# Performance work log

Measured on AMD Instinct MI355X. Metric: run time of the kernel, lower is better.

The kernel has to match this reference:

```python
import jax, jax.numpy as jnp
import numpy as np

K_NEAREST = 5
EPS = 1e-6


def setup_inputs() -> dict:
    key = jax.random.key(0)
    k1, k2, k3 = jax.random.split(key, 3)
    N_Q, N_DB, D_OUT, D_AUX = 4096, 65536, 32, 32
    return {
        "embedding_features": jax.random.normal(k1, (N_Q, D_OUT), dtype=jnp.float32),
        "db_embedding": jax.random.normal(k2, (N_DB, D_OUT), dtype=jnp.float32),
        "auxiliary_features": jax.random.normal(k3, (N_DB, D_AUX), dtype=jnp.float32),
    }


def reference(embedding_features, db_embedding, auxiliary_features):
    d_out = embedding_features.shape[-1]
    q = embedding_features.reshape(-1, d_out)          # [Nq, D]
    db = db_embedding.reshape(-1, d_out)               # [Ndb, D]

    # Euclidean cdist via the expanded quadratic form (same math as torch.cdist p=2).
    q_sq = jnp.sum(q * q, axis=1, keepdims=True)       # [Nq, 1]
    db_sq = jnp.sum(db * db, axis=1)[None, :]          # [1, Ndb]
    dist_sq = q_sq + db_sq - 2.0 * (q @ db.T)          # [Nq, Ndb]
    distances = jnp.sqrt(jnp.maximum(dist_sq, 0.0))

    # k smallest distances == k largest of negated distances.
    neg_top, nearest_indices = jax.lax.top_k(-distances, K_NEAREST)  # [Nq, k]
    nearest_distances = -neg_top                                      # [Nq, k]

    aux = auxiliary_features.reshape(-1, auxiliary_features.shape[-1])
    nearest_aux = aux[nearest_indices]                 # [Nq, k, Daux]

    weights = 1.0 / (nearest_distances + EPS)
    weights = weights / jnp.sum(weights, axis=1, keepdims=True)

    return jnp.sum(nearest_aux * weights[..., None], axis=1)  # [Nq, Daux]
```

## Files before the change

kernel.cpp:

```cpp
#include <hip/hip_runtime.h>
#include <math.h>

#define N_Q   4096
#define N_DB  65536
#define DIM   32
#define KNN   5
#define NC    64
#define CH    (N_DB / NC)
#define NSUB  32
#define NCAND (NC * 6)
#define BIAS  256.0f

typedef _Float16 half8  __attribute__((ext_vector_type(8)));
typedef __fp16   fp16x2 __attribute__((ext_vector_type(2)));
typedef float floatx16  __attribute__((ext_vector_type(16)));

union H8  { half8 h; uint4 u4; unsigned u[4]; };
union F16 { floatx16 v; float4 q4[4]; unsigned w[16]; };
union HU  { fp16x2 h2; unsigned u; };

__device__ __forceinline__ unsigned cvt2(float a, float b) {
    HU t; t.h2 = __builtin_amdgcn_cvt_pkrtz(a, b);
    return t.u;
}

__device__ __forceinline__ void gl4(uint4& d, unsigned long long a) {
    asm volatile("global_load_dwordx4 %0, %1, off" : "=v"(d) : "v"(a) : "memory");
}
__device__ __forceinline__ void gl4_1024(uint4& d, unsigned long long a) {
    asm volatile("global_load_dwordx4 %0, %1, off offset:1024" : "=v"(d) : "v"(a) : "memory");
}
__device__ __forceinline__ void gl1(unsigned& d, unsigned long long a) {
    asm volatile("global_load_dword %0, %1, off" : "=v"(d) : "v"(a) : "memory");
}
#define VMWAIT6 do { asm volatile("s_waitcnt vmcnt(6)" ::: "memory"); \
                     __builtin_amdgcn_sched_barrier(0); } while (0)

__global__ __launch_bounds__(256) void k_prep(const float* __restrict__ DB,
                                              uint4* __restrict__ DBh,
                                              unsigned* __restrict__ DBn) {
    int p = blockIdx.x * 256 + threadIdx.x;
    const float4* src = (const float4*)(DB + (size_t)p * DIM);
    float4 f[8]; float s = 0.f;
#pragma unroll
    for (int j = 0; j < 8; ++j) {
        f[j] = src[j];
        s += f[j].x * f[j].x + f[j].y * f[j].y + f[j].z * f[j].z + f[j].w * f[j].w;
    }
    float v  = BIAS - 0.5f * s;
    float hi = (float)(__fp16)v;
    float lo = v - hi;
    DBn[p] = cvt2(hi, lo);
    int t = p >> 5, r = p & 31;
#pragma unroll
    for (int gi = 0; gi < 4; ++gi) {
        uint4 g;
        g.x = cvt2(f[2 * gi].x, f[2 * gi].y);
        g.y = cvt2(f[2 * gi].z, f[2 * gi].w);
        g.z = cvt2(f[2 * gi + 1].x, f[2 * gi + 1].y);
        g.w = cvt2(f[2 * gi + 1].z, f[2 * gi + 1].w);
        DBh[(size_t)t * 128 + gi * 32 + r] = g;
    }
}

__global__ __launch_bounds__(256, 4) void k_scan(const float* __restrict__ Q,
                                                 const uint4* __restrict__ DBh,
                                                 const unsigned* __restrict__ DBn,
                                                 unsigned* __restrict__ cand) {
    const int tid = threadIdx.x, lane = tid & 63, w = tid >> 6;
    const int h = lane >> 5, row = lane & 31;
    const int chunk = blockIdx.x & (NC - 1);
    const int qb    = blockIdx.x >> 6;
    const int q     = qb * 128 + w * 32 + row;
    const int pbase = chunk * CH;

    const float* qp = Q + (size_t)q * DIM;
    float4 qa = *(const float4*)(qp + h * 8);
    float4 qb4 = *(const float4*)(qp + h * 8 + 4);
    float4 qc = *(const float4*)(qp + 16 + h * 8);
    float4 qd = *(const float4*)(qp + 16 + h * 8 + 4);
    H8 b1, b2, b3;
    b1.u[0] = cvt2(qa.x, qa.y);   b1.u[1] = cvt2(qa.z, qa.w);
    b1.u[2] = cvt2(qb4.x, qb4.y); b1.u[3] = cvt2(qb4.z, qb4.w);
    b2.u[0] = cvt2(qc.x, qc.y);   b2.u[1] = cvt2(qc.z, qc.w);
    b2.u[2] = cvt2(qd.x, qd.y);   b2.u[3] = cvt2(qd.z, qd.w);
    b3.u[0] = (h == 0) ? cvt2(1.f, 1.f) : 0u;
    b3.u[1] = 0u; b3.u[2] = 0u; b3.u[3] = 0u;
    const unsigned hmask = (h == 0) ? 0xFFFFFFFFu : 0u;

    unsigned maskv;
    asm("v_mov_b32 %0, 0xFFFFFC00" : "=v"(maskv));

    const unsigned long long abase_u =
        (unsigned long long)(DBh + (size_t)(pbase >> 5) * 128 + h * 32 + row);
    const unsigned long long nbase_u =
        (unsigned long long)(DBn + pbase + row);

    floatx16 zc;
#pragma unroll
    for (int r = 0; r < 16; ++r) zc[r] = 0.f;

    float tk[6];
#pragma unroll
    for (int r = 0; r < 6; ++r) tk[r] = 0.f;

    constexpr int ROWC[16] = {0,1,2,3, 8,9,10,11, 16,17,18,19, 24,25,26,27};

    auto compute = [&](const H8& A1, const H8& A2, unsigned A3u, const int s) {
        H8 a3;
        a3.u[0] = A3u & hmask;
        a3.u[1] = 0u; a3.u[2] = 0u; a3.u[3] = 0u;
        floatx16 acc = __builtin_amdgcn_mfma_f32_32x32x16_f16(a3.h, b3.h, zc, 0, 0, 0);
        acc = __builtin_amdgcn_mfma_f32_32x32x16_f16(A1.h, b1.h, acc, 0, 0, 0);
        acc = __builtin_amdgcn_mfma_f32_32x32x16_f16(A2.h, b2.h, acc, 0, 0, 0);
        F16 pk; pk.v = acc;
        const int meta = s << 5;
        float p[16];
#pragma unroll
        for (int r = 0; r < 16; ++r)
            p[r] = __uint_as_float((pk.w[r] & maskv) | (unsigned)(meta | ROWC[r]));
        float hi8[8], lo8[8];
#pragma unroll
        for (int i = 0; i < 8; ++i) { hi8[i] = fmaxf(p[2*i], p[2*i+1]); lo8[i] = fminf(p[2*i], p[2*i+1]); }
        float H4[4], L4[4];
#pragma unroll
        for (int i = 0; i < 4; ++i) {
            H4[i] = fmaxf(hi8[2*i], hi8[2*i+1]);
            L4[i] = fmaxf(fmaxf(lo8[2*i], lo8[2*i+1]), fminf(hi8[2*i], hi8[2*i+1]));
        }
        float H2[2], L2[2];
#pragma unroll
        for (int i = 0; i < 2; ++i) {
            H2[i] = fmaxf(H4[2*i], H4[2*i+1]);
            L2[i] = fmaxf(fmaxf(L4[2*i], L4[2*i+1]), fminf(H4[2*i], H4[2*i+1]));
        }
        float c1 = fmaxf(H2[0], H2[1]);
        float c2 = fmaxf(fmaxf(L2[0], L2[1]), fminf(H2[0], H2[1]));
        {
            float m01 = fminf(tk[0], c1), m02 = fminf(tk[1], c1);
            float m03 = fminf(tk[2], c1), m04 = fminf(tk[3], c1);
            float m05 = fminf(tk[4], c1);
            float m12 = fminf(tk[0], c2), m13 = fminf(tk[1], c2);
            float m14 = fminf(tk[2], c2), m15 = fminf(tk[3], c2);
            tk[0] = fmaxf(tk[0], c1);
            tk[1] = fmaxf(fmaxf(tk[1], m01), c2);
            tk[2] = fmaxf(fmaxf(tk[2], m02), m12);
            tk[3] = fmaxf(fmaxf(tk[3], m03), m13);
            tk[4] = fmaxf(fmaxf(tk[4], m04), m14);
            tk[5] = fmaxf(fmaxf(tk[5], m05), m15);
        }
    };

    auto LD = [&](H8& x1, H8& x2, unsigned& x3, const int s) {
        const unsigned long long a = abase_u + (unsigned long long)s * 2048ull;
        gl4(x1.u4, a);
        gl4_1024(x2.u4, a);
        gl1(x3, nbase_u + (unsigned long long)s * 128ull);
    };

    H8 sA1, sA2, sB1, sB2, sC1, sC2, sD1, sD2;
    unsigned nA, nB, nC, nD;
    LD(sA1, sA2, nA, 0);
    LD(sB1, sB2, nB, 1);
    for (int s = 0; s < NSUB; s += 4) {
        LD(sC1, sC2, nC, s + 2);
        VMWAIT6; compute(sA1, sA2, nA, s);
        LD(sD1, sD2, nD, s + 3);
        VMWAIT6; compute(sB1, sB2, nB, s + 1);
        LD(sA1, sA2, nA, s + 4);
        VMWAIT6; compute(sC1, sC2, nC, s + 2);
        LD(sB1, sB2, nB, s + 5);
        VMWAIT6; compute(sD1, sD2, nD, s + 3);
    }

#pragma unroll
    for (int r = 0; r < 6; ++r)
        tk[r] = __uint_as_float(__float_as_uint(tk[r]) | (unsigned)(h << 2));

    float other[6];
#pragma unroll
    for (int i = 0; i < 6; ++i) other[i] = __shfl_xor(tk[i], 32, 64);
#pragma unroll
    for (int i = 0; i < 6; ++i) {
        float val = other[i];
#pragma unroll
        for (int j = 0; j < 6; ++j) { float mx = fmaxf(tk[j], val); val = fminf(tk[j], val); tk[j] = mx; }
    }
    if (h == 0) {
        unsigned* dst = cand + ((size_t)q * NC + chunk) * 6;
#pragma unroll
        for (int r = 0; r < 6; ++r) dst[r] = __float_as_uint(tk[r]);
    }
}

__global__ __launch_bounds__(256) void k_merge(const float* __restrict__ Q,
                                               const float* __restrict__ DB,
                                               const float* __restrict__ AUX,
                                               const unsigned* __restrict__ cand,
                                               float* __restrict__ out) {
    const int tid = threadIdx.x, lane = tid & 63, w = tid >> 6;
    const int q = blockIdx.x * 4 + w;

    const unsigned* cq = cand + (size_t)q * NCAND + (size_t)lane * 6;
    float cur[6];
#pragma unroll
    for (int r = 0; r < 6; ++r) cur[r] = __uint_as_float(cq[r]);

    float wv[12]; int wl[12];
#pragma unroll
    for (int r = 0; r < 12; ++r) {
        float bv = cur[0]; int bl = lane;
#pragma unroll
        for (int off = 32; off >= 1; off >>= 1) {
            float ov = __shfl_xor(bv, off, 64);
            int   ol = __shfl_xor(bl, off, 64);
            if (ov > bv || (ov == bv && ol < bl)) { bv = ov; bl = ol; }
        }
        wv[r] = bv; wl[r] = bl;
        if (bl == lane) {
#pragma unroll
            for (int s = 0; s < 5; ++s) cur[s] = cur[s + 1];
            cur[5] = -1.f;
        }
    }

    float dist = 1e30f; int dbi = 0x7fffffff;
    if (lane < 12) {
        unsigned u = __float_as_uint(wv[lane]) & 1023u;
        dbi = wl[lane] * CH + (int)u;
        const float4* dp = (const float4*)(DB + (size_t)dbi * DIM);
        const float4* qp = (const float4*)(Q + (size_t)q * DIM);
        float dot = 0.f, qs = 0.f, ds = 0.f;
#pragma unroll
        for (int j = 0; j < DIM / 4; ++j) {
            float4 a = qp[j], d = dp[j];
            dot += a.x * d.x + a.y * d.y + a.z * d.z + a.w * d.w;
            qs  += a.x * a.x + a.y * a.y + a.z * a.z + a.w * a.w;
            ds  += d.x * d.x + d.y * d.y + d.z * d.z + d.w * d.w;
        }
        dist = sqrtf(fmaxf(qs + ds - 2.f * dot, 0.f));
    }
    float wd[KNN]; int wi[KNN];
#pragma unroll
    for (int r = 0; r < KNN; ++r) {
        float bd = dist; int bi = dbi;
#pragma unroll
        for (int off = 32; off >= 1; off >>= 1) {
            float od = __shfl_xor(bd, off, 64);
            int   oi = __shfl_xor(bi, off, 64);
            if (od < bd || (od == bd && oi < bi)) { bd = od; bi = oi; }
        }
        wd[r] = bd; wi[r] = bi;
        if (dist == bd && dbi == bi) dist = 1e30f;
    }
    float ww[KNN], W = 0.f;
#pragma unroll
    for (int r = 0; r < KNN; ++r) { ww[r] = 1.f / (wd[r] + 1e-6f); W += ww[r]; }
    if (lane < DIM) {
        float o = 0.f;
#pragma unroll
        for (int r = 0; r < KNN; ++r) o += ww[r] * AUX[(size_t)wi[r] * DIM + lane];
        out[(size_t)q * DIM + lane] = o / W;
    }
}

extern "C" void kernel_launch(void* const* d_in, const int* in_sizes, int n_in,
                              void* d_out, int out_size, void* d_ws, size_t ws_size,
                              hipStream_t stream) {
    const float* Q   = (const float*)d_in[0];
    const float* DB  = (const float*)d_in[1];
    const float* AUX = (const float*)d_in[2];
    float* out = (float*)d_out;

    char* ws = (char*)d_ws;
    uint4*    DBh = (uint4*)ws;                         ws += (size_t)(N_DB / 32) * 128 * 16;
    unsigned* DBn = (unsigned*)ws;                      ws += (size_t)N_DB * 4;
    unsigned* cand = (unsigned*)ws;

    k_prep<<<N_DB / 256, 256, 0, stream>>>(DB, DBh, DBn);
    k_scan<<<(N_Q / 128) * NC, 256, 0, stream>>>(Q, DBh, DBn, cand);
    k_merge<<<N_Q / 4, 256, 0, stream>>>(Q, DB, AUX, cand, out);
}
```

Before: 139.9 us.

## Hand-write top-2 merge in inline asm and shrink load pipeline depth

```diff
diff --git a/kernel.cpp b/kernel.cpp
--- a/kernel.cpp
+++ b/kernel.cpp
@@ -33,7 +33,7 @@
 __device__ __forceinline__ void gl1(unsigned& d, unsigned long long a) {
     asm volatile("global_load_dword %0, %1, off" : "=v"(d) : "v"(a) : "memory");
 }
-#define VMWAIT6 do { asm volatile("s_waitcnt vmcnt(6)" ::: "memory"); \
+#define VMWAIT3 do { asm volatile("s_waitcnt vmcnt(3)" ::: "memory"); \
                      __builtin_amdgcn_sched_barrier(0); } while (0)
 
 __global__ __launch_bounds__(256) void k_prep(const float* __restrict__ DB,
@@ -114,41 +114,74 @@
         acc = __builtin_amdgcn_mfma_f32_32x32x16_f16(A1.h, b1.h, acc, 0, 0, 0);
         acc = __builtin_amdgcn_mfma_f32_32x32x16_f16(A2.h, b2.h, acc, 0, 0, 0);
         F16 pk; pk.v = acc;
-        const int meta = s << 5;
-        float p[16];
+        const unsigned meta = (unsigned)(s << 5);
+        unsigned p[16];
 #pragma unroll
         for (int r = 0; r < 16; ++r)
-            p[r] = __uint_as_float((pk.w[r] & maskv) | (unsigned)(meta | ROWC[r]));
-        float hi8[8], lo8[8];
-#pragma unroll
-        for (int i = 0; i < 8; ++i) { hi8[i] = fmaxf(p[2*i], p[2*i+1]); lo8[i] = fminf(p[2*i], p[2*i+1]); }
-        float H4[4], L4[4];
-#pragma unroll
-        for (int i = 0; i < 4; ++i) {
-            H4[i] = fmaxf(hi8[2*i], hi8[2*i+1]);
-            L4[i] = fmaxf(fmaxf(lo8[2*i], lo8[2*i+1]), fminf(hi8[2*i], hi8[2*i+1]));
-        }
-        float H2[2], L2[2];
-#pragma unroll
-        for (int i = 0; i < 2; ++i) {
-            H2[i] = fmaxf(H4[2*i], H4[2*i+1]);
-            L2[i] = fmaxf(fmaxf(L4[2*i], L4[2*i+1]), fminf(H4[2*i], H4[2*i+1]));
-        }
-        float c1 = fmaxf(H2[0], H2[1]);
-        float c2 = fmaxf(fmaxf(L2[0], L2[1]), fminf(H2[0], H2[1]));
-        {
-            float m01 = fminf(tk[0], c1), m02 = fminf(tk[1], c1);
-            float m03 = fminf(tk[2], c1), m04 = fminf(tk[3], c1);
-            float m05 = fminf(tk[4], c1);
-            float m12 = fminf(tk[0], c2), m13 = fminf(tk[1], c2);
-            float m14 = fminf(tk[2], c2), m15 = fminf(tk[3], c2);
-            tk[0] = fmaxf(tk[0], c1);
-            tk[1] = fmaxf(fmaxf(tk[1], m01), c2);
-            tk[2] = fmaxf(fmaxf(tk[2], m02), m12);
-            tk[3] = fmaxf(fmaxf(tk[3], m03), m13);
-            tk[4] = fmaxf(fmaxf(tk[4], m04), m14);
-            tk[5] = fmaxf(fmaxf(tk[5], m05), m15);
-        }
+            p[r] = (pk.w[r] & maskv) | (meta | (unsigned)ROWC[r]);
+        float q0, q1, q2, q3, T0, T1, T2, T3, U0, U1, U2, U3;
+        asm(
+            "v_max_f32 %[q0], %[p0], %[p1]\n\t"
+            "v_min_f32 %[q1], %[p0], %[p1]\n\t"
+            "v_max_f32 %[q2], %[p2], %[p3]\n\t"
+            "v_min_f32 %[q3], %[p2], %[p3]\n\t"
+            "v_max_f32 %[T0], %[q0], %[q2]\n\t"
+            "v_min_f32 %[U0], %[q0], %[q2]\n\t"
+            "v_max3_f32 %[U0], %[q1], %[q3], %[U0]\n\t"
+            "v_max_f32 %[q0], %[p4], %[p5]\n\t"
+            "v_min_f32 %[q1], %[p4], %[p5]\n\t"
+            "v_max_f32 %[q2], %[p6], %[p7]\n\t"
+            "v_min_f32 %[q3], %[p6], %[p7]\n\t"
+            "v_max_f32 %[T1], %[q0], %[q2]\n\t"
+            "v_min_f32 %[U1], %[q0], %[q2]\n\t"
+            "v_max3_f32 %[U1], %[q1], %[q3], %[U1]\n\t"
+            "v_max_f32 %[q0], %[p8], %[p9]\n\t"
+            "v_min_f32 %[q1], %[p8], %[p9]\n\t"
+            "v_max_f32 %[q2], %[p10], %[p11]\n\t"
+            "v_min_f32 %[q3], %[p10], %[p11]\n\t"
+            "v_max_f32 %[T2], %[q0], %[q2]\n\t"
+            "v_min_f32 %[U2], %[q0], %[q2]\n\t"
+            "v_max3_f32 %[U2], %[q1], %[q3], %[U2]\n\t"
+            "v_max_f32 %[q0], %[p12], %[p13]\n\t"
+            "v_min_f32 %[q1], %[p12], %[p13]\n\t"
+            "v_max_f32 %[q2], %[p14], %[p15]\n\t"
+            "v_min_f32 %[q3], %[p14], %[p15]\n\t"
+            "v_max_f32 %[T3], %[q0], %[q2]\n\t"
+            "v_min_f32 %[U3], %[q0], %[q2]\n\t"
+            "v_max3_f32 %[U3], %[q1], %[q3], %[U3]\n\t"
+            "v_max_f32 %[q0], %[T0], %[T1]\n\t"
+            "v_min_f32 %[q1], %[T0], %[T1]\n\t"
+            "v_max3_f32 %[q2], %[U0], %[U1], %[q1]\n\t"
+            "v_max_f32 %[q1], %[T2], %[T3]\n\t"
+            "v_min_f32 %[q3], %[T2], %[T3]\n\t"
+            "v_max3_f32 %[T0], %[U2], %[U3], %[q3]\n\t"
+            "v_max_f32 %[T1], %[q0], %[q1]\n\t"
+            "v_min_f32 %[T2], %[q0], %[q1]\n\t"
+            "v_max3_f32 %[T3], %[q2], %[T0], %[T2]\n\t"
+            "v_min_f32 %[q0], %[tk0], %[T1]\n\t"
+            "v_min_f32 %[q1], %[tk1], %[T1]\n\t"
+            "v_min_f32 %[q2], %[tk2], %[T1]\n\t"
+            "v_min_f32 %[q3], %[tk3], %[T1]\n\t"
+            "v_min_f32 %[U0], %[tk4], %[T1]\n\t"
+            "v_min_f32 %[U1], %[tk0], %[T3]\n\t"
+            "v_min_f32 %[U2], %[tk1], %[T3]\n\t"
+            "v_min_f32 %[U3], %[tk2], %[T3]\n\t"
+            "v_min_f32 %[T0], %[tk3], %[T3]\n\t"
+            "v_max_f32 %[tk0], %[tk0], %[T1]\n\t"
+            "v_max3_f32 %[tk1], %[tk1], %[q0], %[T3]\n\t"
+            "v_max3_f32 %[tk2], %[tk2], %[q1], %[U1]\n\t"
+            "v_max3_f32 %[tk3], %[tk3], %[q2], %[U2]\n\t"
+            "v_max3_f32 %[tk4], %[tk4], %[q3], %[U3]\n\t"
+            "v_max3_f32 %[tk5], %[tk5], %[U0], %[T0]"
+            : [tk0]"+v"(tk[0]), [tk1]"+v"(tk[1]), [tk2]"+v"(tk[2]),
+              [tk3]"+v"(tk[3]), [tk4]"+v"(tk[4]), [tk5]"+v"(tk[5]),
+              [q0]"=&v"(q0), [q1]"=&v"(q1), [q2]"=&v"(q2), [q3]"=&v"(q3),
+              [T0]"=&v"(T0), [T1]"=&v"(T1), [T2]"=&v"(T2), [T3]"=&v"(T3),
+              [U0]"=&v"(U0), [U1]"=&v"(U1), [U2]"=&v"(U2), [U3]"=&v"(U3)
+            : [p0]"v"(p[0]),  [p1]"v"(p[1]),  [p2]"v"(p[2]),  [p3]"v"(p[3]),
+              [p4]"v"(p[4]),  [p5]"v"(p[5]),  [p6]"v"(p[6]),  [p7]"v"(p[7]),
+              [p8]"v"(p[8]),  [p9]"v"(p[9]),  [p10]"v"(p[10]), [p11]"v"(p[11]),
+              [p12]"v"(p[12]), [p13]"v"(p[13]), [p14]"v"(p[14]), [p15]"v"(p[15]));
     };
 
     auto LD = [&](H8& x1, H8& x2, unsigned& x3, const int s) {
@@ -158,19 +191,14 @@
         gl1(x3, nbase_u + (unsigned long long)s * 128ull);
     };
 
-    H8 sA1, sA2, sB1, sB2, sC1, sC2, sD1, sD2;
-    unsigned nA, nB, nC, nD;
+    H8 sA1, sA2, sB1, sB2;
+    unsigned nA, nB;
     LD(sA1, sA2, nA, 0);
-    LD(sB1, sB2, nB, 1);
-    for (int s = 0; s < NSUB; s += 4) {
-        LD(sC1, sC2, nC, s + 2);
-        VMWAIT6; compute(sA1, sA2, nA, s);
-        LD(sD1, sD2, nD, s + 3);
-        VMWAIT6; compute(sB1, sB2, nB, s + 1);
-        LD(sA1, sA2, nA, s + 4);
-        VMWAIT6; compute(sC1, sC2, nC, s + 2);
-        LD(sB1, sB2, nB, s + 5);
-        VMWAIT6; compute(sD1, sD2, nD, s + 3);
+    for (int s = 0; s < NSUB; s += 2) {
+        LD(sB1, sB2, nB, s + 1);
+        VMWAIT3; compute(sA1, sA2, nA, s);
+        LD(sA1, sA2, nA, s + 2);
+        VMWAIT3; compute(sB1, sB2, nB, s + 1);
     }
 
 #pragma unroll
```

Result: faster. 132.9 us, median of 2 (-5.0%).
